# Kernel tuning notes

Measured on AMD Instinct MI355X. Metric: run time of the kernel, lower is better.

Reference implementation:

```python
import jax, jax.numpy as jnp
import numpy as np

V = 100000  # vocab size
D = 128     # embedding dim
N = 1000000 # number of (context, target) pairs

def setup_inputs() -> dict:
    key = jax.random.key(0)
    k1, k2, k3, k4 = jax.random.split(key, 4)
    # Original inits cxtEmbeddings to zeros; use small random values so the
    # output is non-degenerate for correctness testing.
    bound = 0.5 / D
    cxt_weight = jax.random.uniform(k1, (V, D), jnp.float32, -bound, bound)
    tgt_weight = jax.random.uniform(k2, (V, D), jnp.float32, -bound, bound)
    context_idxs = jax.random.randint(k3, (N,), 0, V, dtype=jnp.int64)
    target_idxs = jax.random.randint(k4, (N,), 0, V, dtype=jnp.int64)
    return {
        "context_idxs": context_idxs,
        "target_idxs": target_idxs,
        "cxt_weight": cxt_weight,
        "tgt_weight": tgt_weight,
    }

def reference(context_idxs, target_idxs, cxt_weight, tgt_weight):
    # Gather embeddings: [N, D]
    context_vectors = cxt_weight[context_idxs]
    target_vectors = tgt_weight[target_idxs]
    # diagonal(C @ T.T) == row-wise dot product; compute it fused to avoid O(N^2 D)
    inner_products = jnp.sum(context_vectors * target_vectors, axis=-1, keepdims=True)  # [N, 1]
    return inner_products
```

## Files before the change

### kernel.cpp

```cpp
#include <hip/hip_runtime.h>
#include <hip/hip_bf16.h>
#include <hip/hip_fp16.h>


#define D 128

typedef _Float16 half8_t __attribute__((ext_vector_type(8)));

__global__ __launch_bounds__(256) void convert_fp16_kernel(
    const float* __restrict__ cxt_w, const float* __restrict__ tgt_w,
    _Float16* __restrict__ cxt_h, _Float16* __restrict__ tgt_h,
    int elems_per_table)
{
    const int per_table_thr = elems_per_table >> 3;
    const int tid = blockIdx.x * blockDim.x + threadIdx.x;

    const float* src;
    _Float16* dst;
    int off;
    if (tid < per_table_thr) {
        src = cxt_w; dst = cxt_h; off = tid << 3;
    } else if (tid < 2 * per_table_thr) {
        src = tgt_w; dst = tgt_h; off = (tid - per_table_thr) << 3;
    } else {
        return;
    }

    const float4 a = *reinterpret_cast<const float4*>(src + off);
    const float4 b = *reinterpret_cast<const float4*>(src + off + 4);
    half8_t h;
    h[0] = (_Float16)a.x; h[1] = (_Float16)a.y;
    h[2] = (_Float16)a.z; h[3] = (_Float16)a.w;
    h[4] = (_Float16)b.x; h[5] = (_Float16)b.y;
    h[6] = (_Float16)b.z; h[7] = (_Float16)b.w;
    *reinterpret_cast<half8_t*>(dst + off) = h;
}

__global__ __launch_bounds__(256) void gather_dot_h_kernel(
    const int* __restrict__ ctx_idx,
    const int* __restrict__ tgt_idx,
    const _Float16* __restrict__ cxt_h,
    const _Float16* __restrict__ tgt_h,
    float* __restrict__ out,
    int n)
{
    const int lane = threadIdx.x & 15;
    const long long g = ((long long)blockIdx.x * blockDim.x + threadIdx.x) >> 4;
    const int p0 = (int)(g << 2);
    if (p0 >= n) return;

    if (p0 + 4 <= n) {
        const int4 ci4 = *reinterpret_cast<const int4*>(ctx_idx + p0);
        const int4 ti4 = *reinterpret_cast<const int4*>(tgt_idx + p0);
        const int ci[4] = {ci4.x, ci4.y, ci4.z, ci4.w};
        const int ti[4] = {ti4.x, ti4.y, ti4.z, ti4.w};

        half8_t c[4], t[4];
        #pragma unroll
        for (int u = 0; u < 4; ++u) {
            c[u] = *reinterpret_cast<const half8_t*>(cxt_h + (size_t)ci[u] * D + lane * 8);
            t[u] = *reinterpret_cast<const half8_t*>(tgt_h + (size_t)ti[u] * D + lane * 8);
        }

        float p[4];
        #pragma unroll
        for (int u = 0; u < 4; ++u) {
            float s = 0.f;
            #pragma unroll
            for (int k = 0; k < 8; ++k)
                s = fmaf((float)c[u][k], (float)t[u][k], s);
            p[u] = s;
        }
        #pragma unroll
        for (int u = 0; u < 4; ++u) {
            p[u] += __shfl_xor(p[u], 8);
            p[u] += __shfl_xor(p[u], 4);
            p[u] += __shfl_xor(p[u], 2);
            p[u] += __shfl_xor(p[u], 1);
        }
        if (lane == 0)
            *reinterpret_cast<float4*>(out + p0) = make_float4(p[0], p[1], p[2], p[3]);
    } else {
        for (int u = 0; u < 4 && p0 + u < n; ++u) {
            const int pi = p0 + u;
            const int cidx = ctx_idx[pi];
            const int tidx = tgt_idx[pi];
            const half8_t c = *reinterpret_cast<const half8_t*>(cxt_h + (size_t)cidx * D + lane * 8);
            const half8_t t = *reinterpret_cast<const half8_t*>(tgt_h + (size_t)tidx * D + lane * 8);
            float s = 0.f;
            #pragma unroll
            for (int k = 0; k < 8; ++k)
                s = fmaf((float)c[k], (float)t[k], s);
            s += __shfl_xor(s, 8);
            s += __shfl_xor(s, 4);
            s += __shfl_xor(s, 2);
            s += __shfl_xor(s, 1);
            if (lane == 0) out[pi] = s;
        }
    }
}

__global__ __launch_bounds__(256) void gather_dot_f32_kernel(
    const int* __restrict__ ctx_idx, const int* __restrict__ tgt_idx,
    const float* __restrict__ cxt_w, const float* __restrict__ tgt_w,
    float* __restrict__ out, int n)
{
    const int lane = threadIdx.x & 31;
    const long long g = ((long long)blockIdx.x * blockDim.x + threadIdx.x) >> 5;
    const int pair = (int)g;
    if (pair >= n) return;
    const int ci = ctx_idx[pair];
    const int ti = tgt_idx[pair];
    const float4 c = reinterpret_cast<const float4*>(cxt_w + (size_t)ci * D)[lane];
    const float4 t = reinterpret_cast<const float4*>(tgt_w + (size_t)ti * D)[lane];
    float s = c.x * t.x;
    s = fmaf(c.y, t.y, s);
    s = fmaf(c.z, t.z, s);
    s = fmaf(c.w, t.w, s);
    s += __shfl_xor(s, 16);
    s += __shfl_xor(s, 8);
    s += __shfl_xor(s, 4);
    s += __shfl_xor(s, 2);
    s += __shfl_xor(s, 1);
    if (lane == 0) out[pair] = s;
}

extern "C" void kernel_launch(void* const* d_in, const int* in_sizes, int n_in,
                              void* d_out, int out_size, void* d_ws, size_t ws_size,
                              hipStream_t stream) {
    const int*   ctx_idx = (const int*)d_in[0];
    const int*   tgt_idx = (const int*)d_in[1];
    const float* cxt_w   = (const float*)d_in[2];
    const float* tgt_w   = (const float*)d_in[3];
    float*       out     = (float*)d_out;

    const int n = in_sizes[0];
    const int elems = in_sizes[2];
    const size_t need = (size_t)elems * 2 * sizeof(_Float16);

    if (ws_size >= need) {
        _Float16* cxt_h = (_Float16*)d_ws;
        _Float16* tgt_h = cxt_h + elems;

        const int conv_threads = (elems >> 3) * 2;
        const int conv_grid = (conv_threads + 255) / 256;
        convert_fp16_kernel<<<conv_grid, 256, 0, stream>>>(
            cxt_w, tgt_w, cxt_h, tgt_h, elems);

        const int pairs_per_block = (256 / 16) * 4;
        const int grid = (n + pairs_per_block - 1) / pairs_per_block;
        gather_dot_h_kernel<<<grid, 256, 0, stream>>>(
            ctx_idx, tgt_idx, cxt_h, tgt_h, out, n);
    } else {
        const int grid = (n + 7) / 8;
        gather_dot_f32_kernel<<<grid, 256, 0, stream>>>(
            ctx_idx, tgt_idx, cxt_w, tgt_w, out, n);
    }
}
```

Before: 198.3 us.

## Bucket-sort pairs by context index before gathering to improve locality

Adds a histogram, scan and atomic scatter pass that buckets the (context, target, id) triples by the high bits of the context index. The gather-dot kernel then walks the sorted order with blocks interleaved across eight chunks and writes results back through the original ids. The aim is better cache reuse of context-table rows, which are fp16-converted into the workspace first. The cost is three extra kernel launches, extra index traffic, atomic contention in the scatter, and scattered output stores.

```diff
diff --git a/kernel.cpp b/kernel.cpp
--- a/kernel.cpp
+++ b/kernel.cpp
@@ -4,14 +4,20 @@
 
 
 #define D 128
+#define BSHIFT 7
+#define NB 1024
 
 typedef _Float16 half8_t __attribute__((ext_vector_type(8)));
 
 __global__ __launch_bounds__(256) void convert_fp16_kernel(
     const float* __restrict__ cxt_w, const float* __restrict__ tgt_w,
     _Float16* __restrict__ cxt_h, _Float16* __restrict__ tgt_h,
-    int elems_per_table)
-{
+    int elems_per_table, unsigned* __restrict__ hist, int conv_grid)
+{
+    if ((int)blockIdx.x == conv_grid) {
+        for (int i = threadIdx.x; i < NB; i += 256) hist[i] = 0u;
+        return;
+    }
     const int per_table_thr = elems_per_table >> 3;
     const int tid = blockIdx.x * blockDim.x + threadIdx.x;
 
@@ -36,22 +42,74 @@
     *reinterpret_cast<half8_t*>(dst + off) = h;
 }
 
-__global__ __launch_bounds__(256) void gather_dot_h_kernel(
-    const int* __restrict__ ctx_idx,
-    const int* __restrict__ tgt_idx,
-    const _Float16* __restrict__ cxt_h,
-    const _Float16* __restrict__ tgt_h,
-    float* __restrict__ out,
-    int n)
-{
+__global__ __launch_bounds__(256) void hist_kernel(
+    const int* __restrict__ ctx, int n, unsigned* __restrict__ hist)
+{
+    __shared__ unsigned lh[NB];
+    for (int i = threadIdx.x; i < NB; i += 256) lh[i] = 0u;
+    __syncthreads();
+    for (long long i = blockIdx.x * 256ll + threadIdx.x; i < n;
+         i += (long long)gridDim.x * 256)
+        atomicAdd(&lh[ctx[i] >> BSHIFT], 1u);
+    __syncthreads();
+    for (int i = threadIdx.x; i < NB; i += 256) {
+        unsigned v = lh[i];
+        if (v) atomicAdd(&hist[i], v);
+    }
+}
+
+__global__ __launch_bounds__(1024) void scan_kernel(
+    const unsigned* __restrict__ hist, unsigned* __restrict__ cursor)
+{
+    __shared__ unsigned s[NB];
+    const int t = threadIdx.x;
+    const unsigned own = hist[t];
+    s[t] = own;
+    __syncthreads();
+    #pragma unroll
+    for (int off = 1; off < NB; off <<= 1) {
+        unsigned add = (t >= off) ? s[t - off] : 0u;
+        __syncthreads();
+        s[t] += add;
+        __syncthreads();
+    }
+    cursor[t] = s[t] - own;
+}
+
+__global__ __launch_bounds__(256) void scatter_kernel(
+    const int* __restrict__ ctx, const int* __restrict__ tgt, int n,
+    unsigned* __restrict__ cursor,
+    int* __restrict__ sctx, int* __restrict__ stgt, int* __restrict__ sid)
+{
+    const long long i = blockIdx.x * 256ll + threadIdx.x;
+    if (i >= n) return;
+    const int c = ctx[i];
+    const int t = tgt[i];
+    const unsigned pos = atomicAdd(&cursor[c >> BSHIFT], 1u);
+    sctx[pos] = c;
+    stgt[pos] = t;
+    sid[pos] = (int)i;
+}
+
+__global__ __launch_bounds__(256) void gather_dot_sorted_kernel(
+    const int* __restrict__ sctx, const int* __restrict__ stgt,
+    const int* __restrict__ sid,
+    const _Float16* __restrict__ cxt_h, const _Float16* __restrict__ tgt_h,
+    float* __restrict__ out, int n, int nlogical)
+{
+    const int chunks = (nlogical + 7) >> 3;
+    const int lb = (int)(blockIdx.x & 7) * chunks + (int)(blockIdx.x >> 3);
+    if (lb >= nlogical) return;
+
     const int lane = threadIdx.x & 15;
-    const long long g = ((long long)blockIdx.x * blockDim.x + threadIdx.x) >> 4;
-    const int p0 = (int)(g << 2);
+    const int grp  = threadIdx.x >> 4;
+    const int p0 = lb * 64 + grp * 4;
     if (p0 >= n) return;
 
     if (p0 + 4 <= n) {
-        const int4 ci4 = *reinterpret_cast<const int4*>(ctx_idx + p0);
-        const int4 ti4 = *reinterpret_cast<const int4*>(tgt_idx + p0);
+        const int4 ci4 = *reinterpret_cast<const int4*>(sctx + p0);
+        const int4 ti4 = *reinterpret_cast<const int4*>(stgt + p0);
+        const int4 id4 = *reinterpret_cast<const int4*>(sid + p0);
         const int ci[4] = {ci4.x, ci4.y, ci4.z, ci4.w};
         const int ti[4] = {ti4.x, ti4.y, ti4.z, ti4.w};
 
@@ -78,13 +136,17 @@
             p[u] += __shfl_xor(p[u], 2);
             p[u] += __shfl_xor(p[u], 1);
         }
-        if (lane == 0)
-            *reinterpret_cast<float4*>(out + p0) = make_float4(p[0], p[1], p[2], p[3]);
+        if (lane == 0) {
+            out[id4.x] = p[0];
+            out[id4.y] = p[1];
+            out[id4.z] = p[2];
+            out[id4.w] = p[3];
+        }
     } else {
         for (int u = 0; u < 4 && p0 + u < n; ++u) {
             const int pi = p0 + u;
-            const int cidx = ctx_idx[pi];
-            const int tidx = tgt_idx[pi];
+            const int cidx = sctx[pi];
+            const int tidx = stgt[pi];
             const half8_t c = *reinterpret_cast<const half8_t*>(cxt_h + (size_t)cidx * D + lane * 8);
             const half8_t t = *reinterpret_cast<const half8_t*>(tgt_h + (size_t)tidx * D + lane * 8);
             float s = 0.f;
@@ -95,8 +157,33 @@
             s += __shfl_xor(s, 4);
             s += __shfl_xor(s, 2);
             s += __shfl_xor(s, 1);
-            if (lane == 0) out[pi] = s;
-        }
+            if (lane == 0) out[sid[pi]] = s;
+        }
+    }
+}
+
+__global__ __launch_bounds__(256) void gather_dot_h_kernel(
+    const int* __restrict__ ctx_idx, const int* __restrict__ tgt_idx,
+    const _Float16* __restrict__ cxt_h, const _Float16* __restrict__ tgt_h,
+    float* __restrict__ out, int n)
+{
+    const int lane = threadIdx.x & 15;
+    const long long g = ((long long)blockIdx.x * blockDim.x + threadIdx.x) >> 4;
+    const int p0 = (int)(g << 2);
+    if (p0 >= n) return;
+    for (int u = 0; u < 4 && p0 + u < n; ++u) {
+        const int pi = p0 + u;
+        const half8_t c = *reinterpret_cast<const half8_t*>(cxt_h + (size_t)ctx_idx[pi] * D + lane * 8);
+        const half8_t t = *reinterpret_cast<const half8_t*>(tgt_h + (size_t)tgt_idx[pi] * D + lane * 8);
+        float s = 0.f;
+        #pragma unroll
+        for (int k = 0; k < 8; ++k)
+            s = fmaf((float)c[k], (float)t[k], s);
+        s += __shfl_xor(s, 8);
+        s += __shfl_xor(s, 4);
+        s += __shfl_xor(s, 2);
+        s += __shfl_xor(s, 1);
+        if (lane == 0) out[pi] = s;
     }
 }
 
@@ -109,10 +196,8 @@
     const long long g = ((long long)blockIdx.x * blockDim.x + threadIdx.x) >> 5;
     const int pair = (int)g;
     if (pair >= n) return;
-    const int ci = ctx_idx[pair];
-    const int ti = tgt_idx[pair];
-    const float4 c = reinterpret_cast<const float4*>(cxt_w + (size_t)ci * D)[lane];
-    const float4 t = reinterpret_cast<const float4*>(tgt_w + (size_t)ti * D)[lane];
+    const float4 c = reinterpret_cast<const float4*>(cxt_w + (size_t)ctx_idx[pair] * D)[lane];
+    const float4 t = reinterpret_cast<const float4*>(tgt_w + (size_t)tgt_idx[pair] * D)[lane];
     float s = c.x * t.x;
     s = fmaf(c.y, t.y, s);
     s = fmaf(c.z, t.z, s);
@@ -136,24 +221,45 @@
 
     const int n = in_sizes[0];
     const int elems = in_sizes[2];
-    const size_t need = (size_t)elems * 2 * sizeof(_Float16);
-
-    if (ws_size >= need) {
+
+    const size_t tab_bytes = (size_t)elems * sizeof(_Float16);
+    const size_t need_fp16 = 2 * tab_bytes;
+    const size_t need_sorted = need_fp16 + 2 * NB * sizeof(unsigned) + 3 * (size_t)n * sizeof(int) + 256;
+
+    if (ws_size >= need_sorted) {
+        char* p = (char*)d_ws;
+        _Float16* cxt_h = (_Float16*)p;            p += tab_bytes;
+        _Float16* tgt_h = (_Float16*)p;            p += tab_bytes;
+        unsigned* hist   = (unsigned*)p;           p += NB * sizeof(unsigned);
+        unsigned* cursor = (unsigned*)p;           p += NB * sizeof(unsigned);
+        int* sctx = (int*)p;                       p += (size_t)n * sizeof(int);
+        int* stgt = (int*)p;                       p += (size_t)n * sizeof(int);
+        int* sid  = (int*)p;
+
+        const int conv_grid = ((elems >> 3) * 2 + 255) / 256;
+        convert_fp16_kernel<<<conv_grid + 1, 256, 0, stream>>>(
+            cxt_w, tgt_w, cxt_h, tgt_h, elems, hist, conv_grid);
+
+        hist_kernel<<<128, 256, 0, stream>>>(ctx_idx, n, hist);
+        scan_kernel<<<1, 1024, 0, stream>>>(hist, cursor);
+        scatter_kernel<<<(n + 255) / 256, 256, 0, stream>>>(
+            ctx_idx, tgt_idx, n, cursor, sctx, stgt, sid);
+
+        const int nlogical = (n + 63) / 64;
+        const int chunks = (nlogical + 7) >> 3;
+        gather_dot_sorted_kernel<<<chunks * 8, 256, 0, stream>>>(
+            sctx, stgt, sid, cxt_h, tgt_h, out, n, nlogical);
+    } else if (ws_size >= need_fp16) {
         _Float16* cxt_h = (_Float16*)d_ws;
         _Float16* tgt_h = cxt_h + elems;
-
-        const int conv_threads = (elems >> 3) * 2;
-        const int conv_grid = (conv_threads + 255) / 256;
+        const int conv_grid = ((elems >> 3) * 2 + 255) / 256;
         convert_fp16_kernel<<<conv_grid, 256, 0, stream>>>(
-            cxt_w, tgt_w, cxt_h, tgt_h, elems);
-
+            cxt_w, tgt_w, cxt_h, tgt_h, elems, (unsigned*)d_ws, conv_grid + 1);
         const int pairs_per_block = (256 / 16) * 4;
-        const int grid = (n + pairs_per_block - 1) / pairs_per_block;
-        gather_dot_h_kernel<<<grid, 256, 0, stream>>>(
+        gather_dot_h_kernel<<<(n + pairs_per_block - 1) / pairs_per_block, 256, 0, stream>>>(
             ctx_idx, tgt_idx, cxt_h, tgt_h, out, n);
     } else {
-        const int grid = (n + 7) / 8;
-        gather_dot_f32_kernel<<<grid, 256, 0, stream>>>(
+        gather_dot_f32_kernel<<<(n + 7) / 8, 256, 0, stream>>>(
             ctx_idx, tgt_idx, cxt_w, tgt_w, out, n);
     }
 }
```

New measurement: 434.3 us. +119.0%, slower.
